# Kernel optimization log

Hardware: AMD Instinct MI355X
Metric: run time of the kernel (lower is better)

The kernel has to match this reference:

```python
import jax, jax.numpy as jnp
import numpy as np

HEAD_SIZE = 128
LAMBDA_INIT = 0.8
FILL = 1e-09  # the module fills masked positions with 1e-9 (not -inf); reproduce faithfully


def setup_inputs() -> dict:
    key = jax.random.key(0)
    ks = jax.random.split(key, 12)
    B, T, C = 8, 2048, 1024
    q = jax.random.normal(ks[0], (B, T, C), dtype=jnp.float32)
    k = jax.random.normal(ks[1], (B, T, C), dtype=jnp.float32)
    v = jax.random.normal(ks[2], (B, T, C), dtype=jnp.float32)
    pad_mask = jax.random.randint(ks[3], (B, T), 0, 2, dtype=jnp.int32)
    scale = 1.0 / np.sqrt(C)
    Wq = jax.random.normal(ks[4], (C, 2 * HEAD_SIZE), dtype=jnp.float32) * scale
    Wk = jax.random.normal(ks[5], (C, 2 * HEAD_SIZE), dtype=jnp.float32) * scale
    Wv = jax.random.normal(ks[6], (C, HEAD_SIZE), dtype=jnp.float32) * scale
    lq1 = jax.random.normal(ks[7], (HEAD_SIZE,), dtype=jnp.float32)
    lk1 = jax.random.normal(ks[8], (HEAD_SIZE,), dtype=jnp.float32)
    lq2 = jax.random.normal(ks[9], (HEAD_SIZE,), dtype=jnp.float32)
    lk2 = jax.random.normal(ks[10], (HEAD_SIZE,), dtype=jnp.float32)
    return {"q": q, "k": k, "v": v, "pad_mask": pad_mask,
            "Wq": Wq, "Wk": Wk, "Wv": Wv,
            "lq1": lq1, "lk1": lk1, "lq2": lq2, "lk2": lk2}


def reference(q, k, v, pad_mask, Wq, Wk, Wv, lq1, lk1, lq2, lk2):
    B, T_q, C = q.shape
    T_k = k.shape[1]
    Q = q @ Wq                      # [B, Tq, 2*hs]
    K = k @ Wk                      # [B, Tk, 2*hs]
    V = v @ Wv                      # [B, Tk, ho]
    Q1, Q2 = jnp.split(Q, 2, axis=-1)
    K1, K2 = jnp.split(K, 2, axis=-1)
    s1 = jnp.einsum("bqd,bkd->bqk", Q1, K1)
    s2 = jnp.einsum("bqd,bkd->bqk", Q2, K2)
    # causal mask: tril(ones, diagonal=1) == 0 -> fill (note diagonal=1, one lookahead)
    causal_fill = jnp.tril(jnp.ones((T_q, T_k), dtype=bool), 1) == False
    s1 = jnp.where(causal_fill[None], FILL, s1)
    s2 = jnp.where(causal_fill[None], FILL, s2)
    # pad mask broadcast over the KEY axis per query row (as in original)
    pad_fill = (pad_mask == 1)[:, :, None]  # [B, Tq, 1]
    s1 = jnp.where(pad_fill, FILL, s1)
    s2 = jnp.where(pad_fill, FILL, s2)
    scale = HEAD_SIZE ** (-0.5)
    lbd = jnp.exp(jnp.dot(lq1, lk1)) - jnp.exp(jnp.dot(lq2, lk2)) + LAMBDA_INIT
    attn = jax.nn.softmax(s1 * scale, axis=-1) - lbd * jax.nn.softmax(s2 * scale, axis=-1)
    return attn @ V                 # [B, Tq, ho]
```

## Files before the change

### kernel.cpp

```cpp
#include <hip/hip_runtime.h>
#include <math.h>


#define T_SEQ 2048
#define NB 8
#define CDIM 1024
#define HS 128

constexpr float SCALE = 0.08838834764831845f;

typedef float f32x4 __attribute__((ext_vector_type(4)));
typedef __bf16 bf16x8 __attribute__((ext_vector_type(8)));
typedef unsigned int u32;

#define MFMA16 __builtin_amdgcn_mfma_f32_16x16x32_bf16

__device__ __forceinline__ void gld16(const void* g, void* l) {
  __builtin_amdgcn_global_load_lds(
      (const __attribute__((address_space(1))) u32*)g,
      (__attribute__((address_space(3))) u32*)l, 16, 0, 0);
}

__device__ __forceinline__ void wg_barrier_lds() {
  asm volatile("s_waitcnt lgkmcnt(0)" ::: "memory");
  __builtin_amdgcn_s_barrier();
  __builtin_amdgcn_sched_barrier(0);
}

__device__ __forceinline__ bf16x8 cvt8(f32x4 lo, f32x4 hi) {
  bf16x8 r;
  r[0] = (__bf16)lo.x; r[1] = (__bf16)lo.y; r[2] = (__bf16)lo.z; r[3] = (__bf16)lo.w;
  r[4] = (__bf16)hi.x; r[5] = (__bf16)hi.y; r[6] = (__bf16)hi.z; r[7] = (__bf16)hi.w;
  return r;
}

__global__ __launch_bounds__(128) void lambda_kernel(
    const float* __restrict__ lq1, const float* __restrict__ lk1,
    const float* __restrict__ lq2, const float* __restrict__ lk2,
    float* __restrict__ lbd) {
  __shared__ float r1[128], r2[128];
  int t = threadIdx.x;
  r1[t] = lq1[t] * lk1[t];
  r2[t] = lq2[t] * lk2[t];
  __syncthreads();
  for (int s = 64; s > 0; s >>= 1) {
    if (t < s) { r1[t] += r1[t + s]; r2[t] += r2[t + s]; }
    __syncthreads();
  }
  if (t == 0) *lbd = expf(r1[0]) - expf(r2[0]) + 0.8f;
}

__global__ __launch_bounds__(256) void pack_w(
    const float* __restrict__ Wq, const float* __restrict__ Wk,
    const float* __restrict__ Wv, __bf16* __restrict__ Wp) {
  int nt = blockIdx.x;
  const float* W; int colbase, N;
  if (nt < 16)      { W = Wq; colbase = nt * 16;        N = 256; }
  else if (nt < 32) { W = Wk; colbase = (nt - 16) * 16; N = 256; }
  else              { W = Wv; colbase = (nt - 32) * 16; N = 128; }
  int tid = threadIdx.x;
#pragma unroll
  for (int i = 0; i < 8; ++i) {
    int u = tid + 256 * i;
    int ks = u >> 6, lane = u & 63;
    int l15 = lane & 15, quad = lane >> 4;
    bf16x8 pk;
#pragma unroll
    for (int j = 0; j < 8; ++j)
      pk[j] = (__bf16)W[(size_t)(ks * 32 + quad * 8 + j) * N + colbase + l15];
    *(bf16x8*)(Wp + ((size_t)(nt * 32 + ks) * 64 + lane) * 8) = pk;
  }
}

template<int NT, int NTG>
__device__ __forceinline__ void proj_body(
    const float* __restrict__ Ablk, const __bf16* __restrict__ Wp,
    __bf16* __restrict__ outp, __bf16* __restrict__ Vt,
    int rows0, char* smem) {
  float*  sA = (float*)smem;
  __bf16* sB = (__bf16*)(smem + 32768);
  const int tid = threadIdx.x;
  const int lane = tid & 63, wave = tid >> 6;
  const int l15 = lane & 15, quad = lane >> 4;
  const int arow = lane >> 3;
  const int ac16 = (lane & 7) ^ arow;

  f32x4 acc0[NT], acc1[NT];
#pragma unroll
  for (int j = 0; j < NT; ++j) {
    acc0[j] = (f32x4){0.f, 0.f, 0.f, 0.f};
    acc1[j] = (f32x4){0.f, 0.f, 0.f, 0.f};
  }

  auto stage_ks = [&](int ks, int buf) {
    const float* gA = Ablk + ks * 32;
    float* lA = sA + buf * 4096;
#pragma unroll
    for (int i = 0; i < 4; ++i) {
      int li = wave * 4 + i;
      gld16(gA + (size_t)(li * 8 + arow) * CDIM + ac16 * 4, lA + li * 256);
    }
    __bf16* lB = sB + buf * 8192;
#pragma unroll
    for (int i = 0; i < 4; ++i) {
      int ntl = wave * 4 + i;
      if (ntl < NT)
        gld16(Wp + ((size_t)((NTG + ntl) * 32 + ks) * 64 + lane) * 8,
              lB + ntl * 512);
    }
  };

  stage_ks(0, 0);
  for (int ks = 0; ks < 32; ++ks) {
    const int buf = ks & 1;
    __syncthreads();
    const float* lA = sA + buf * 4096;
    int r0 = wave * 32 + l15;
    f32x4 lo0 = *(const f32x4*)(lA + r0 * 32 + (((quad * 2)     ^ (l15 & 7)) * 4));
    f32x4 hi0 = *(const f32x4*)(lA + r0 * 32 + (((quad * 2 + 1) ^ (l15 & 7)) * 4));
    bf16x8 af0 = cvt8(lo0, hi0);
    int r1 = r0 + 16;
    f32x4 lo1 = *(const f32x4*)(lA + r1 * 32 + (((quad * 2)     ^ (l15 & 7)) * 4));
    f32x4 hi1 = *(const f32x4*)(lA + r1 * 32 + (((quad * 2 + 1) ^ (l15 & 7)) * 4));
    bf16x8 af1 = cvt8(lo1, hi1);
    if (ks < 31) stage_ks(ks + 1, buf ^ 1);
    const __bf16* lB = sB + buf * 8192;
#pragma unroll
    for (int nt = 0; nt < NT; ++nt) {
      bf16x8 bf = *(const bf16x8*)(lB + nt * 512 + lane * 8);
      acc0[nt] = MFMA16(af0, bf, acc0[nt], 0, 0, 0);
      acc1[nt] = MFMA16(af1, bf, acc1[nt], 0, 0, 0);
    }
  }

  __syncthreads();
  __bf16* tile = (__bf16*)smem;
  constexpr int N = NT * 16;
#pragma unroll
  for (int half = 0; half < (NT >> 3); ++half) {
#pragma unroll
    for (int ntl = 0; ntl < 8; ++ntl) {
      f32x4 a0 = acc0[half * 8 + ntl];
      f32x4 a1 = acc1[half * 8 + ntl];
#pragma unroll
      for (int r = 0; r < 4; ++r) {
        tile[(wave * 32 + quad * 4 + r) * 136 + ntl * 16 + l15] = (__bf16)a0[r];
        tile[(wave * 32 + 16 + quad * 4 + r) * 136 + ntl * 16 + l15] = (__bf16)a1[r];
      }
    }
    __syncthreads();
#pragma unroll
    for (int i = 0; i < 8; ++i) {
      int u = tid + 256 * i;
      int row = u >> 4, c8 = u & 15;
      bf16x8 val = *(const bf16x8*)(tile + row * 136 + c8 * 8);
      *(bf16x8*)(outp + (size_t)(rows0 + row) * N + half * 128 + c8 * 8) = val;
    }
    if constexpr (NT == 8) {
      int b = rows0 >> 11, t0 = rows0 & 2047;
#pragma unroll
      for (int i = 0; i < 8; ++i) {
        int u = tid + 256 * i;
        int tc = u & 15, c = u >> 4;
        bf16x8 pk;
#pragma unroll
        for (int j = 0; j < 8; ++j) pk[j] = tile[(tc * 8 + j) * 136 + c];
        *(bf16x8*)(Vt + ((size_t)(b * 128 + c)) * T_SEQ + t0 + tc * 8) = pk;
      }
    }
    __syncthreads();
  }
}

__global__ __launch_bounds__(256, 2) void proj_mfma(
    const float* __restrict__ qin, const float* __restrict__ kin,
    const float* __restrict__ vin, const __bf16* __restrict__ Wp,
    __bf16* __restrict__ Qo, __bf16* __restrict__ Ko,
    __bf16* __restrict__ Vo, __bf16* __restrict__ Vt) {
  __shared__ char smem[65536];
  const int blk = blockIdx.x;
  const int rows0 = (blk & 127) * 128;
  if (blk < 128)
    proj_body<16, 0>(qin + (size_t)rows0 * CDIM, Wp, Qo, nullptr, rows0, smem);
  else if (blk < 256)
    proj_body<16, 16>(kin + (size_t)rows0 * CDIM, Wp, Ko, nullptr, rows0, smem);
  else
    proj_body<8, 32>(vin + (size_t)rows0 * CDIM, Wp, Vo, Vt, rows0, smem);
}

__global__ __launch_bounds__(128) void vcsum_a(const __bf16* __restrict__ V,
                                               float* __restrict__ csum) {
  int blk = blockIdx.x; int b = blk >> 4, ch = blk & 15;
  int c = threadIdx.x;
  const __bf16* vp = V + ((size_t)b * T_SEQ + ch * 128) * HS + c;
  float s = 0.f;
#pragma unroll 4
  for (int t = 0; t < 128; ++t) s += (float)vp[(size_t)t * HS];
  csum[(size_t)blk * HS + c] = s;
}

__global__ __launch_bounds__(128) void vcsum_b(const __bf16* __restrict__ V,
                                               const float* __restrict__ csum,
                                               float* __restrict__ cum) {
  int blk = blockIdx.x; int b = blk >> 4, ch = blk & 15;
  int c = threadIdx.x;
  float run = 0.f;
  for (int j = 0; j < ch; ++j) run += csum[(size_t)(b * 16 + j) * HS + c];
  const __bf16* vp = V + ((size_t)b * T_SEQ + ch * 128) * HS + c;
  float* cp = cum + ((size_t)b * (T_SEQ + 1) + ch * 128) * HS + c;
  if (ch == 0) cp[0] = 0.f;
#pragma unroll 4
  for (int t = 0; t < 128; ++t) {
    run += (float)vp[(size_t)t * HS];
    cp[(size_t)(t + 1) * HS] = run;
  }
}

__global__ __launch_bounds__(512, 2) void attn_mfma(
    const __bf16* __restrict__ Q, const __bf16* __restrict__ K,
    const __bf16* __restrict__ Vt, const float* __restrict__ cum,
    const int* __restrict__ pad, const float* __restrict__ lbdp,
    float* __restrict__ out) {
  __shared__ __bf16 sQ[32 * 264];
  __shared__ __bf16 sP[2][2][32 * 136];
  __shared__ float zb[2][32][64];
  __shared__ float zfin[2][32];

  const int tid = threadIdx.x;
  const int lane = tid & 63, wave = tid >> 6;
  const int wm = wave >> 2, wk = wave & 3;
  const int l15 = lane & 15, quad = lane >> 4;

  const int p = blockIdx.x;
  const int b = p & 7;
  const int ti = 63 - (p >> 3);
  const int q0 = ti * 32;
  const float lbd = *lbdp;
  const __bf16* Qb = Q + (size_t)b * T_SEQ * 256;
  const __bf16* Kb = K + (size_t)b * T_SEQ * 256;
  const __bf16* Vtb = Vt + (size_t)b * HS * T_SEQ;
  const float* cumb = cum + (size_t)b * (T_SEQ + 1) * HS;
  const float pc = (1.f - lbd) * (1.f / (float)T_SEQ);

  const int lastkey = q0 + 32;
  const int nkt = (min(lastkey, T_SEQ - 1) >> 7) + 1;

  bf16x8 kf[2][2][4];
  bf16x8 vf[2][4];
  auto loadK = [&](int k0) {
#pragma unroll
    for (int mat = 0; mat < 2; ++mat) {
      const __bf16* kp = Kb + (size_t)(k0 + wk * 32 + l15) * 256 + mat * 128 + quad * 8;
#pragma unroll
      for (int s = 0; s < 4; ++s) {
        kf[mat][0][s] = *(const bf16x8*)(kp + s * 32);
        kf[mat][1][s] = *(const bf16x8*)(kp + 16 * 256 + s * 32);
      }
    }
  };
  auto loadV = [&](int k0) {
#pragma unroll
    for (int nt = 0; nt < 2; ++nt)
#pragma unroll
      for (int ks = 0; ks < 4; ++ks)
        vf[nt][ks] = *(const bf16x8*)(Vtb + (size_t)(wk * 32 + nt * 16 + l15) * T_SEQ +
                                      k0 + ks * 32 + quad * 8);
  };
  loadK(0);
  loadV(0);

#pragma unroll
  for (int i = 0; i < 2; ++i) {
    int c = tid + 512 * i;
    int row = c >> 5, c16 = c & 31;
    *(f32x4*)(&sQ[row * 264 + c16 * 8]) =
        *(const f32x4*)(Qb + (size_t)(q0 + row) * 256 + c16 * 8);
  }
  wg_barrier_lds();

  bf16x8 qf[2][4];
  {
    const int row = wm * 16 + l15;
#pragma unroll
    for (int pl = 0; pl < 2; ++pl)
#pragma unroll
      for (int s = 0; s < 4; ++s)
        qf[pl][s] = *(const bf16x8*)(&sQ[row * 264 + pl * 128 + s * 32 + quad * 8]);
  }

  f32x4 O[2][2];
#pragma unroll
  for (int i = 0; i < 2; ++i)
#pragma unroll
    for (int j = 0; j < 2; ++j) O[i][j] = (f32x4){0.f, 0.f, 0.f, 0.f};
  float z[2][4] = {};

  for (int kt = 0; kt < nkt; ++kt) {
    const int k0 = kt << 7;
    const bool needmask = (k0 + 127 > q0 + 1);
    const int buf = kt & 1;

    f32x4 S[2][2];
#pragma unroll
    for (int mat = 0; mat < 2; ++mat) {
      S[mat][0] = (f32x4){0.f, 0.f, 0.f, 0.f};
      S[mat][1] = (f32x4){0.f, 0.f, 0.f, 0.f};
#pragma unroll
      for (int s = 0; s < 4; ++s) {
        S[mat][0] = MFMA16(qf[mat][s], kf[mat][0][s], S[mat][0], 0, 0, 0);
        S[mat][1] = MFMA16(qf[mat][s], kf[mat][1][s], S[mat][1], 0, 0, 0);
      }
    }
    if (kt + 1 < nkt) loadK(k0 + 128);

    const int rowl = wm * 16 + quad * 4;
#pragma unroll
    for (int mat = 0; mat < 2; ++mat)
#pragma unroll
      for (int nt = 0; nt < 2; ++nt) {
        const int keyg = k0 + wk * 32 + nt * 16 + l15;
#pragma unroll
        for (int r = 0; r < 4; ++r) {
          float pv;
          if (needmask) {
            int rowg = q0 + rowl + r;
            pv = (keyg <= rowg + 1) ? __expf(S[mat][nt][r] * SCALE) : 0.f;
          } else {
            pv = __expf(S[mat][nt][r] * SCALE);
          }
          z[mat][r] += pv;
          sP[buf][mat][(rowl + r) * 136 + wk * 32 + nt * 16 + l15] = (__bf16)pv;
        }
      }
    wg_barrier_lds();

#pragma unroll
    for (int ks = 0; ks < 4; ++ks) {
      bf16x8 pf0 = *(const bf16x8*)(&sP[buf][0][(wm * 16 + l15) * 136 + ks * 32 + quad * 8]);
      bf16x8 pf1 = *(const bf16x8*)(&sP[buf][1][(wm * 16 + l15) * 136 + ks * 32 + quad * 8]);
#pragma unroll
      for (int nt = 0; nt < 2; ++nt) {
        O[0][nt] = MFMA16(pf0, vf[nt][ks], O[0][nt], 0, 0, 0);
        O[1][nt] = MFMA16(pf1, vf[nt][ks], O[1][nt], 0, 0, 0);
      }
    }
    if (kt + 1 < nkt) loadV(k0 + 128);
  }

#pragma unroll
  for (int mat = 0; mat < 2; ++mat)
#pragma unroll
    for (int r = 0; r < 4; ++r)
      zb[mat][wm * 16 + quad * 4 + r][wk * 16 + l15] = z[mat][r];
  __syncthreads();
  if (tid < 64) {
    int mat = tid >> 5, row = tid & 31;
    float s = 0.f;
#pragma unroll
    for (int j = 0; j < 64; ++j) s += zb[mat][row][(j + tid) & 63];
    zfin[mat][row] = s;
  }
  __syncthreads();

#pragma unroll
  for (int r = 0; r < 4; ++r) {
    const int rowl = wm * 16 + quad * 4 + r;
    const int rowg = q0 + rowl;
    const int nallow = min(rowg + 2, T_SEQ);
    const float nmask = (float)(T_SEQ - nallow);
    const float Z1 = zfin[0][rowl] + nmask;
    const float Z2 = zfin[1][rowl] + nmask;
    const float i1 = 1.f / Z1, i2 = lbd / Z2;
    const float tc = i1 - i2;
    const bool isp = (pad[b * T_SEQ + rowg] == 1);
#pragma unroll
    for (int nt = 0; nt < 2; ++nt) {
      const int col = wk * 32 + nt * 16 + l15;
      const float ct = cumb[(size_t)T_SEQ * HS + col];
      const float cn = cumb[(size_t)nallow * HS + col];
      float val = isp ? (pc * ct)
                      : (O[0][nt][r] * i1 - O[1][nt][r] * i2 + tc * (ct - cn));
      out[((size_t)b * T_SEQ + rowg) * HS + col] = val;
    }
  }
}

extern "C" void kernel_launch(void* const* d_in, const int* in_sizes, int n_in,
                              void* d_out, int out_size, void* d_ws, size_t ws_size,
                              hipStream_t stream) {
  (void)in_sizes; (void)n_in; (void)out_size; (void)ws_size;
  const float* q   = (const float*)d_in[0];
  const float* k   = (const float*)d_in[1];
  const float* v   = (const float*)d_in[2];
  const int*   pm  = (const int*)d_in[3];
  const float* Wq  = (const float*)d_in[4];
  const float* Wk  = (const float*)d_in[5];
  const float* Wv  = (const float*)d_in[6];
  const float* lq1 = (const float*)d_in[7];
  const float* lk1 = (const float*)d_in[8];
  const float* lq2 = (const float*)d_in[9];
  const float* lk2 = (const float*)d_in[10];
  float* out = (float*)d_out;
  char* ws = (char*)d_ws;

  float*  lbd  = (float*)ws;
  __bf16* Wp   = (__bf16*)(ws + 16);
  __bf16* Qp   = (__bf16*)(ws + 16 + 1310720);
  __bf16* Kp   = Qp + (size_t)NB * T_SEQ * 256;
  __bf16* Vp   = Kp + (size_t)NB * T_SEQ * 256;
  __bf16* Vt   = Vp + (size_t)NB * T_SEQ * HS;
  float*  cum  = (float*)(Vt + (size_t)NB * T_SEQ * HS);
  float*  csum = cum + (size_t)NB * (T_SEQ + 1) * HS;

  lambda_kernel<<<dim3(1), dim3(128), 0, stream>>>(lq1, lk1, lq2, lk2, lbd);
  pack_w<<<dim3(40), dim3(256), 0, stream>>>(Wq, Wk, Wv, Wp);
  proj_mfma<<<dim3(384), dim3(256), 0, stream>>>(q, k, v, Wp, Qp, Kp, Vp, Vt);
  vcsum_a<<<dim3(128), dim3(128), 0, stream>>>(Vp, csum);
  vcsum_b<<<dim3(128), dim3(128), 0, stream>>>(Vp, csum, cum);
  attn_mfma<<<dim3(512), dim3(512), 0, stream>>>(Qp, Kp, Vt, cum, pm, lbd, out);
}
```

Measured before the change: 370.9 us.

## Stage K tiles into swizzled LDS via async loads and shrink key tile

The attention kernel now stages 64-key K tiles into double-buffered, XOR-swizzled shared memory with global_load_lds, replacing per-wave register prefetch of 128-key K tiles. Each wave reads its K fragments from LDS, and V fragments are loaded per iteration. The key tile is halved to 64, so each wave covers 16 keys, and a full barrier is added per iteration. Separately, the V cumulative-sum kernels use 64 chunks of 32 rows instead of 16 of 128 to expose more parallelism. The trade-off is more loop iterations and barriers and higher LDS use, which may lower occupancy, in exchange for lower register pressure and less duplicated K loading.

```diff
diff --git a/kernel.cpp b/kernel.cpp
--- a/kernel.cpp
+++ b/kernel.cpp
@@ -188,29 +188,31 @@
     proj_body<8, 32>(vin + (size_t)rows0 * CDIM, Wp, Vo, Vt, rows0, smem);
 }
 
+#define VCH 64
+#define VCS 32
 __global__ __launch_bounds__(128) void vcsum_a(const __bf16* __restrict__ V,
                                                float* __restrict__ csum) {
-  int blk = blockIdx.x; int b = blk >> 4, ch = blk & 15;
+  int blk = blockIdx.x; int b = blk >> 6, ch = blk & 63;
   int c = threadIdx.x;
-  const __bf16* vp = V + ((size_t)b * T_SEQ + ch * 128) * HS + c;
+  const __bf16* vp = V + ((size_t)b * T_SEQ + ch * VCS) * HS + c;
   float s = 0.f;
 #pragma unroll 4
-  for (int t = 0; t < 128; ++t) s += (float)vp[(size_t)t * HS];
+  for (int t = 0; t < VCS; ++t) s += (float)vp[(size_t)t * HS];
   csum[(size_t)blk * HS + c] = s;
 }
 
 __global__ __launch_bounds__(128) void vcsum_b(const __bf16* __restrict__ V,
                                                const float* __restrict__ csum,
                                                float* __restrict__ cum) {
-  int blk = blockIdx.x; int b = blk >> 4, ch = blk & 15;
+  int blk = blockIdx.x; int b = blk >> 6, ch = blk & 63;
   int c = threadIdx.x;
   float run = 0.f;
-  for (int j = 0; j < ch; ++j) run += csum[(size_t)(b * 16 + j) * HS + c];
-  const __bf16* vp = V + ((size_t)b * T_SEQ + ch * 128) * HS + c;
-  float* cp = cum + ((size_t)b * (T_SEQ + 1) + ch * 128) * HS + c;
+  for (int j = 0; j < ch; ++j) run += csum[(size_t)(b * VCH + j) * HS + c];
+  const __bf16* vp = V + ((size_t)b * T_SEQ + ch * VCS) * HS + c;
+  float* cp = cum + ((size_t)b * (T_SEQ + 1) + ch * VCS) * HS + c;
   if (ch == 0) cp[0] = 0.f;
 #pragma unroll 4
-  for (int t = 0; t < 128; ++t) {
+  for (int t = 0; t < VCS; ++t) {
     run += (float)vp[(size_t)t * HS];
     cp[(size_t)(t + 1) * HS] = run;
   }
@@ -222,7 +224,8 @@
     const int* __restrict__ pad, const float* __restrict__ lbdp,
     float* __restrict__ out) {
   __shared__ __bf16 sQ[32 * 264];
-  __shared__ __bf16 sP[2][2][32 * 136];
+  __shared__ __bf16 sK[2][64 * 256];
+  __shared__ __bf16 sP[2][2][32 * 72];
   __shared__ float zb[2][32][64];
   __shared__ float zfin[2][32];
 
@@ -243,32 +246,20 @@
   const float pc = (1.f - lbd) * (1.f / (float)T_SEQ);
 
   const int lastkey = q0 + 32;
-  const int nkt = (min(lastkey, T_SEQ - 1) >> 7) + 1;
-
-  bf16x8 kf[2][2][4];
-  bf16x8 vf[2][4];
-  auto loadK = [&](int k0) {
-#pragma unroll
-    for (int mat = 0; mat < 2; ++mat) {
-      const __bf16* kp = Kb + (size_t)(k0 + wk * 32 + l15) * 256 + mat * 128 + quad * 8;
-#pragma unroll
-      for (int s = 0; s < 4; ++s) {
-        kf[mat][0][s] = *(const bf16x8*)(kp + s * 32);
-        kf[mat][1][s] = *(const bf16x8*)(kp + 16 * 256 + s * 32);
-      }
+  const int nkt = (min(lastkey, T_SEQ - 1) >> 6) + 1;
+
+  auto stageK = [&](int k0, int sbuf) {
+#pragma unroll
+    for (int i = 0; i < 4; ++i) {
+      int u = i * 512 + tid;
+      int row = u >> 5, c = u & 31;
+      int cg = (c & 24) | ((c ^ row) & 7);
+      gld16(Kb + (size_t)(k0 + row) * 256 + cg * 8,
+            &sK[sbuf][(size_t)(i * 512 + wave * 64) * 8]);
     }
   };
-  auto loadV = [&](int k0) {
-#pragma unroll
-    for (int nt = 0; nt < 2; ++nt)
-#pragma unroll
-      for (int ks = 0; ks < 4; ++ks)
-        vf[nt][ks] = *(const bf16x8*)(Vtb + (size_t)(wk * 32 + nt * 16 + l15) * T_SEQ +
-                                      k0 + ks * 32 + quad * 8);
-  };
-  loadK(0);
-  loadV(0);
-
+
+  stageK(0, 0);
 #pragma unroll
   for (int i = 0; i < 2; ++i) {
     int c = tid + 512 * i;
@@ -276,7 +267,7 @@
     *(f32x4*)(&sQ[row * 264 + c16 * 8]) =
         *(const f32x4*)(Qb + (size_t)(q0 + row) * 256 + c16 * 8);
   }
-  wg_barrier_lds();
+  __syncthreads();
 
   bf16x8 qf[2][4];
   {
@@ -295,56 +286,64 @@
     for (int j = 0; j < 2; ++j) O[i][j] = (f32x4){0.f, 0.f, 0.f, 0.f};
   float z[2][4] = {};
 
+  const int kr = wk * 16 + l15;
+
   for (int kt = 0; kt < nkt; ++kt) {
-    const int k0 = kt << 7;
-    const bool needmask = (k0 + 127 > q0 + 1);
+    const int k0 = kt << 6;
     const int buf = kt & 1;
-
-    f32x4 S[2][2];
+    const bool needmask = (k0 + 63 > q0 + 1);
+
+    bf16x8 vf[2][2];
+#pragma unroll
+    for (int nt = 0; nt < 2; ++nt)
+#pragma unroll
+      for (int ks = 0; ks < 2; ++ks)
+        vf[nt][ks] = *(const bf16x8*)(Vtb + (size_t)(wk * 32 + nt * 16 + l15) * T_SEQ +
+                                      k0 + ks * 32 + quad * 8);
+    if (kt + 1 < nkt) stageK(k0 + 64, buf ^ 1);
+
+    f32x4 S[2];
 #pragma unroll
     for (int mat = 0; mat < 2; ++mat) {
-      S[mat][0] = (f32x4){0.f, 0.f, 0.f, 0.f};
-      S[mat][1] = (f32x4){0.f, 0.f, 0.f, 0.f};
+      S[mat] = (f32x4){0.f, 0.f, 0.f, 0.f};
 #pragma unroll
       for (int s = 0; s < 4; ++s) {
-        S[mat][0] = MFMA16(qf[mat][s], kf[mat][0][s], S[mat][0], 0, 0, 0);
-        S[mat][1] = MFMA16(qf[mat][s], kf[mat][1][s], S[mat][1], 0, 0, 0);
+        int cd = mat * 16 + s * 4 + quad;
+        int slot = (cd & 24) | ((cd ^ kr) & 7);
+        bf16x8 kfrag = *(const bf16x8*)(&sK[buf][(size_t)kr * 256 + slot * 8]);
+        S[mat] = MFMA16(qf[mat][s], kfrag, S[mat], 0, 0, 0);
       }
     }
-    if (kt + 1 < nkt) loadK(k0 + 128);
 
     const int rowl = wm * 16 + quad * 4;
+    const int keyg = k0 + kr;
 #pragma unroll
     for (int mat = 0; mat < 2; ++mat)
 #pragma unroll
-      for (int nt = 0; nt < 2; ++nt) {
-        const int keyg = k0 + wk * 32 + nt * 16 + l15;
-#pragma unroll
-        for (int r = 0; r < 4; ++r) {
-          float pv;
-          if (needmask) {
-            int rowg = q0 + rowl + r;
-            pv = (keyg <= rowg + 1) ? __expf(S[mat][nt][r] * SCALE) : 0.f;
-          } else {
-            pv = __expf(S[mat][nt][r] * SCALE);
-          }
-          z[mat][r] += pv;
-          sP[buf][mat][(rowl + r) * 136 + wk * 32 + nt * 16 + l15] = (__bf16)pv;
+      for (int r = 0; r < 4; ++r) {
+        float pv;
+        if (needmask) {
+          int rowg = q0 + rowl + r;
+          pv = (keyg <= rowg + 1) ? __expf(S[mat][r] * SCALE) : 0.f;
+        } else {
+          pv = __expf(S[mat][r] * SCALE);
         }
+        z[mat][r] += pv;
+        sP[buf][mat][(rowl + r) * 72 + kr] = (__bf16)pv;
       }
     wg_barrier_lds();
 
 #pragma unroll
-    for (int ks = 0; ks < 4; ++ks) {
-      bf16x8 pf0 = *(const bf16x8*)(&sP[buf][0][(wm * 16 + l15) * 136 + ks * 32 + quad * 8]);
-      bf16x8 pf1 = *(const bf16x8*)(&sP[buf][1][(wm * 16 + l15) * 136 + ks * 32 + quad * 8]);
+    for (int ks = 0; ks < 2; ++ks) {
+      bf16x8 pf0 = *(const bf16x8*)(&sP[buf][0][(wm * 16 + l15) * 72 + ks * 32 + quad * 8]);
+      bf16x8 pf1 = *(const bf16x8*)(&sP[buf][1][(wm * 16 + l15) * 72 + ks * 32 + quad * 8]);
 #pragma unroll
       for (int nt = 0; nt < 2; ++nt) {
         O[0][nt] = MFMA16(pf0, vf[nt][ks], O[0][nt], 0, 0, 0);
         O[1][nt] = MFMA16(pf1, vf[nt][ks], O[1][nt], 0, 0, 0);
       }
     }
-    if (kt + 1 < nkt) loadV(k0 + 128);
+    __syncthreads();
   }
 
 #pragma unroll
@@ -415,7 +414,7 @@
   lambda_kernel<<<dim3(1), dim3(128), 0, stream>>>(lq1, lk1, lq2, lk2, lbd);
   pack_w<<<dim3(40), dim3(256), 0, stream>>>(Wq, Wk, Wv, Wp);
   proj_mfma<<<dim3(384), dim3(256), 0, stream>>>(q, k, v, Wp, Qp, Kp, Vp, Vt);
-  vcsum_a<<<dim3(128), dim3(128), 0, stream>>>(Vp, csum);
-  vcsum_b<<<dim3(128), dim3(128), 0, stream>>>(Vp, csum, cum);
+  vcsum_a<<<dim3(512), dim3(128), 0, stream>>>(Vp, csum);
+  vcsum_b<<<dim3(512), dim3(128), 0, stream>>>(Vp, csum, cum);
   attn_mfma<<<dim3(512), dim3(512), 0, stream>>>(Qp, Kp, Vt, cum, pm, lbd, out);
 }
```

Measured after the change: 329.8 us. -11.1%, faster.
